# Optimization experiments

Hardware: AMD Instinct MI355X
Metric: run time of the kernel (lower is better)

The kernel has to match this reference:

```python
import jax, jax.numpy as jnp
import numpy as np

B, C, INTER, H, W = 4, 256, 128, 64, 64
EPS = 1e-5

def conv1x1(x, w, b):
    # x: [B,Cin,H,W], w: [Cout,Cin], b: [Cout]
    return jnp.einsum('bchw,oc->bohw', x, w) + b[None, :, None, None]

def setup_inputs() -> dict:
    key = jax.random.key(0)
    ks = jax.random.split(key, 12)
    sc_in = 1.0 / np.sqrt(C)
    sc_int = 1.0 / np.sqrt(INTER)
    return {
        'x': jax.random.normal(ks[0], (B, C, H, W), dtype=jnp.float32),
        'g_w': jax.random.normal(ks[1], (INTER, C), dtype=jnp.float32) * sc_in,
        'g_b': jax.random.normal(ks[2], (INTER,), dtype=jnp.float32) * 0.01,
        'theta_w': jax.random.normal(ks[3], (INTER, C), dtype=jnp.float32) * sc_in,
        'theta_b': jax.random.normal(ks[4], (INTER,), dtype=jnp.float32) * 0.01,
        'phi_w': jax.random.normal(ks[5], (INTER, C), dtype=jnp.float32) * sc_in,
        'phi_b': jax.random.normal(ks[6], (INTER,), dtype=jnp.float32) * 0.01,
        'w_w': jax.random.normal(ks[7], (C, INTER), dtype=jnp.float32) * sc_int,
        'w_b': jax.random.normal(ks[8], (C,), dtype=jnp.float32) * 0.01,
        'gamma': jax.random.normal(ks[9], (C,), dtype=jnp.float32) * 0.1 + 1.0,
        'beta': jax.random.normal(ks[10], (C,), dtype=jnp.float32) * 0.1,
    }

def reference(x, g_w, g_b, theta_w, theta_b, phi_w, phi_b, w_w, w_b, gamma, beta):
    b, c, h, w = x.shape
    n = h * w
    g_x = conv1x1(x, g_w, g_b).reshape(b, INTER, n).transpose(0, 2, 1)      # [b,n,d]
    theta_x = conv1x1(x, theta_w, theta_b).reshape(b, INTER, n).transpose(0, 2, 1)  # [b,n,d]
    phi_x = conv1x1(x, phi_w, phi_b).reshape(b, INTER, n)                   # [b,d,n]
    f = jnp.einsum('bnd,bdm->bnm', theta_x, phi_x)                          # [b,n,n]
    f_div_c = jax.nn.softmax(f, axis=-1)
    y = jnp.einsum('bnm,bmd->bnd', f_div_c, g_x)                            # [b,n,d]
    y = y.transpose(0, 2, 1).reshape(b, INTER, h, w)                        # [b,d,h,w]
    w_y = conv1x1(y, w_w, w_b)                                              # [b,c,h,w]
    # BatchNorm2d (training mode: batch statistics, biased variance)
    mean = jnp.mean(w_y, axis=(0, 2, 3), keepdims=True)
    var = jnp.var(w_y, axis=(0, 2, 3), keepdims=True)
    bn = (w_y - mean) * jax.lax.rsqrt(var + EPS)
    bn = bn * gamma[None, :, None, None] + beta[None, :, None, None]
    return bn + x
```

## Files before the change

kernel.cpp:

```cpp
#include <hip/hip_runtime.h>

#define B_ 4
#define C_ 256
#define D_ 128
#define N_ 4096
#define BN_ 16384

typedef unsigned short u16t;
typedef _Float16 f16t;
typedef f16t f16x8 __attribute__((ext_vector_type(8)));
typedef f16t f16x4 __attribute__((ext_vector_type(4)));
typedef float f32x4 __attribute__((ext_vector_type(4)));

static __device__ __forceinline__ u16t f2h(float f) {
  f16t h = (f16t)f; u16t u; __builtin_memcpy(&u, &h, 2); return u;
}
static __device__ __forceinline__ float h2f(u16t u) {
  f16t h; __builtin_memcpy(&h, &u, 2); return (float)h;
}

static __device__ __forceinline__ void gld_lds16(const u16t* g, u16t* l) {
  __builtin_amdgcn_global_load_lds(
      (const __attribute__((address_space(1))) void*)g,
      (__attribute__((address_space(3))) void*)l, 16, 0, 0);
}

__global__ __launch_bounds__(256) void prep_w(const float* __restrict__ th_w,
                                              const float* __restrict__ ph_w,
                                              const float* __restrict__ th_b,
                                              const float* __restrict__ ph_b,
                                              const float* __restrict__ g_w,
                                              const float* __restrict__ w_w,
                                              u16t* __restrict__ Wc, u16t* __restrict__ gwc,
                                              u16t* __restrict__ wwc, float* __restrict__ bc,
                                              float* __restrict__ stats) {
  const int idx = blockIdx.x * 256 + threadIdx.x;
  if (idx < 65536) {
    const int j = idx >> 8, c = idx & 255;
    const float v = (j < 128) ? th_w[j * 256 + c] : ph_w[(j - 128) * 256 + c];
    Wc[idx] = f2h(v);
  } else if (idx < 98304) {
    const int i = idx - 65536;
    gwc[i] = f2h(g_w[i]);
  } else if (idx < 131072) {
    const int i = idx - 98304;
    wwc[i] = f2h(w_w[i]);
  } else if (idx < 131328) {
    const int j = idx - 131072;
    bc[j] = (j < 128) ? th_b[j] : ph_b[j - 128];
  } else if (idx < 131840) {
    stats[idx - 131328] = 0.f;
  }
}

__global__ __launch_bounds__(256) void transpose_x(const float* __restrict__ x,
                                                   u16t* __restrict__ xT) {
  __shared__ u16t t[32][33];
  const int b = blockIdx.z, c0 = blockIdx.y * 32, n0 = blockIdx.x * 32;
  const int tid = threadIdx.x;
  {
    const int cl = tid >> 3, n4 = (tid & 7) * 4;
    const float4 v = *(const float4*)(x + ((size_t)b * C_ + c0 + cl) * N_ + n0 + n4);
    t[n4 + 0][cl] = f2h(v.x);
    t[n4 + 1][cl] = f2h(v.y);
    t[n4 + 2][cl] = f2h(v.z);
    t[n4 + 3][cl] = f2h(v.w);
  }
  __syncthreads();
  {
    const int nl = tid >> 3, c4 = (tid & 7) * 4;
    unsigned int lo = (unsigned int)t[nl][c4 + 0] | ((unsigned int)t[nl][c4 + 1] << 16);
    unsigned int hi = (unsigned int)t[nl][c4 + 2] | ((unsigned int)t[nl][c4 + 3] << 16);
    uint2 o; o.x = lo; o.y = hi;
    *(uint2*)(xT + ((size_t)b * N_ + n0 + nl) * C_ + c0 + c4) = o;
  }
}

__global__ __launch_bounds__(256)
void gemm_qkv(const u16t* __restrict__ xT, const u16t* __restrict__ Wc,
              const u16t* __restrict__ gwc, const float* __restrict__ bc,
              const float* __restrict__ g_b, u16t* __restrict__ QKo,
              u16t* __restrict__ Vo) {
  __shared__ __attribute__((aligned(16))) u16t lA[128 * 40];
  __shared__ __attribute__((aligned(16))) u16t lB[128 * 40];
  const int z = blockIdx.z, bx = blockIdx.x;
  const u16t* xTb = xT + (size_t)z * N_ * C_;
  const u16t* A; const u16t* B; u16t* Cb; int ldc, m0, j0, colb;
  const float* bias;
  if (bx < 64) {
    A = xTb; B = Wc; Cb = QKo + (size_t)z * N_ * 256; ldc = 256;
    m0 = (bx >> 1) * 128; j0 = (bx & 1) * 128; bias = bc; colb = 1;
  } else {
    A = gwc; B = xTb; Cb = Vo + (size_t)z * D_ * N_; ldc = N_;
    m0 = 0; j0 = (bx - 64) * 128; bias = g_b; colb = 0;
  }
  const int tid = threadIdx.x, lane = tid & 63, wave = tid >> 6;
  const int quad = lane >> 4, l16 = lane & 15;
  const int wm = wave & 1, wj = wave >> 1;

  const f32x4 zero = {0.f, 0.f, 0.f, 0.f};
  f32x4 acc[4][4];
#pragma unroll
  for (int mi = 0; mi < 4; ++mi)
#pragma unroll
    for (int ji = 0; ji < 4; ++ji) acc[mi][ji] = zero;

  for (int k0 = 0; k0 < 256; k0 += 32) {
#pragma unroll
    for (int rr = 0; rr < 2; ++rr) {
      const int idx = rr * 256 + tid;
      const int row = idx >> 2, sg = idx & 3;
      *(uint4*)&lA[row * 40 + sg * 8] = *(const uint4*)(A + (size_t)(m0 + row) * 256 + k0 + sg * 8);
      *(uint4*)&lB[row * 40 + sg * 8] = *(const uint4*)(B + (size_t)(j0 + row) * 256 + k0 + sg * 8);
    }
    __syncthreads();
    f16x8 af[4], bfr[4];
#pragma unroll
    for (int i = 0; i < 4; ++i)
      af[i] = *(const f16x8*)&lA[(wm * 64 + i * 16 + l16) * 40 + quad * 8];
#pragma unroll
    for (int i = 0; i < 4; ++i)
      bfr[i] = *(const f16x8*)&lB[(wj * 64 + i * 16 + l16) * 40 + quad * 8];
#pragma unroll
    for (int mi = 0; mi < 4; ++mi)
#pragma unroll
      for (int ji = 0; ji < 4; ++ji)
        acc[mi][ji] = __builtin_amdgcn_mfma_f32_16x16x32_f16(af[mi], bfr[ji], acc[mi][ji], 0, 0, 0);
    __syncthreads();
  }

  float cb[4];
  if (colb) {
#pragma unroll
    for (int ji = 0; ji < 4; ++ji) cb[ji] = bias[j0 + wj * 64 + ji * 16 + l16];
  }
#pragma unroll
  for (int mi = 0; mi < 4; ++mi) {
#pragma unroll
    for (int r = 0; r < 4; ++r) {
      const int row = m0 + wm * 64 + mi * 16 + quad * 4 + r;
      const float rb = colb ? 0.f : bias[row];
#pragma unroll
      for (int ji = 0; ji < 4; ++ji) {
        const int col = j0 + wj * 64 + ji * 16 + l16;
        const float v = acc[mi][ji][r] + (colb ? cb[ji] : rb);
        Cb[(size_t)row * ldc + col] = f2h(v);
      }
    }
  }
}

__global__ __launch_bounds__(256, 2)
void attn(const u16t* __restrict__ QK, const u16t* __restrict__ V,
          u16t* __restrict__ On0, u16t* __restrict__ On1, float* __restrict__ ml) {
  const int b = blockIdx.y;
  const int split = blockIdx.z;
  const int n0 = blockIdx.x * 128;
  const int kv0 = split * (N_ / 4);
  const int tid = threadIdx.x, lane = tid & 63, wave = tid >> 6;
  const int quad = lane >> 4, l16 = lane & 15;
  const int x7 = l16 & 7;
  __shared__ __attribute__((aligned(16))) u16t Ks[2][64 * 128];
  __shared__ __attribute__((aligned(16))) u16t Vs[2][128 * 64];
  const u16t* QKb = QK + (size_t)b * N_ * 256;
  const u16t* Vb  = V  + (size_t)b * D_ * N_;

  const int krow_l = lane >> 4, kchunk_l = lane & 15;
  const int vrow_l = lane >> 3, vchunk_l = lane & 7;

  f16x8 qf[2][4];
#pragma unroll
  for (int qi = 0; qi < 2; ++qi) {
    const u16t* qrow = QKb + (size_t)(n0 + wave * 32 + qi * 16 + l16) * 256;
#pragma unroll
    for (int kc = 0; kc < 4; ++kc)
      qf[qi][kc] = *(const f16x8*)(qrow + kc * 32 + quad * 8);
  }

  const f32x4 zero = {0.f, 0.f, 0.f, 0.f};
  f32x4 o[2][8];
#pragma unroll
  for (int qi = 0; qi < 2; ++qi)
#pragma unroll
    for (int db = 0; db < 8; ++db) o[qi][db] = zero;
  float m[2] = {-1e30f, -1e30f}, l[2] = {0.f, 0.f};

#pragma unroll
  for (int i = 0; i < 4; ++i) {
    const int krow = (wave * 4 + i) * 4 + krow_l;
    const int kcl = kchunk_l ^ (krow & 7);
    gld_lds16(QKb + (size_t)(kv0 + krow) * 256 + 128 + kcl * 8,
              &Ks[0][(wave * 4 + i) * 512]);
  }
#pragma unroll
  for (int i = 0; i < 4; ++i) {
    const int vrow = (wave * 4 + i) * 8 + vrow_l;
    const int vcl = vchunk_l ^ (vrow & 7);
    gld_lds16(Vb + (size_t)vrow * N_ + kv0 + vcl * 8,
              &Vs[0][(wave * 4 + i) * 512]);
  }
  __syncthreads();

  int cur = 0;
  for (int it = 0; it < 16; ++it) {
    if (it < 15) {
      const int kvn = kv0 + (it + 1) * 64;
#pragma unroll
      for (int i = 0; i < 4; ++i) {
        const int krow = (wave * 4 + i) * 4 + krow_l;
        const int kcl = kchunk_l ^ (krow & 7);
        gld_lds16(QKb + (size_t)(kvn + krow) * 256 + 128 + kcl * 8,
                  &Ks[cur ^ 1][(wave * 4 + i) * 512]);
      }
#pragma unroll
      for (int i = 0; i < 4; ++i) {
        const int vrow = (wave * 4 + i) * 8 + vrow_l;
        const int vcl = vchunk_l ^ (vrow & 7);
        gld_lds16(Vb + (size_t)vrow * N_ + kvn + vcl * 8,
                  &Vs[cur ^ 1][(wave * 4 + i) * 512]);
      }
    }

    const u16t* KsC = &Ks[cur][0];
    const u16t* VsC = &Vs[cur][0];

    f32x4 s[2][4];
#pragma unroll
    for (int qi = 0; qi < 2; ++qi)
#pragma unroll
      for (int ci = 0; ci < 4; ++ci) s[qi][ci] = zero;
#pragma unroll
    for (int kc = 0; kc < 4; ++kc) {
#pragma unroll
      for (int ci = 0; ci < 4; ++ci) {
        f16x8 kf = *(const f16x8*)&KsC[(ci * 16 + l16) * 128 + (((kc * 4 + quad) ^ x7) << 3)];
        s[0][ci] = __builtin_amdgcn_mfma_f32_16x16x32_f16(kf, qf[0][kc], s[0][ci], 0, 0, 0);
        s[1][ci] = __builtin_amdgcn_mfma_f32_16x16x32_f16(kf, qf[1][kc], s[1][ci], 0, 0, 0);
      }
    }

    float al[2];
    f16x4 pb[2][4];
#pragma unroll
    for (int qi = 0; qi < 2; ++qi) {
      float mx = s[qi][0][0];
#pragma unroll
      for (int ci = 0; ci < 4; ++ci)
#pragma unroll
        for (int r = 0; r < 4; ++r) mx = fmaxf(mx, s[qi][ci][r]);
      mx = fmaxf(mx, __shfl_xor(mx, 16));
      mx = fmaxf(mx, __shfl_xor(mx, 32));
      const float mnew = fmaxf(m[qi], mx);
      al[qi] = __expf(m[qi] - mnew);
      float psum = 0.f;
#pragma unroll
      for (int ci = 0; ci < 4; ++ci) {
#pragma unroll
        for (int r = 0; r < 4; ++r) {
          const float p = __expf(s[qi][ci][r] - mnew);
          psum += p;
          pb[qi][ci][r] = (f16t)p;
        }
      }
      psum += __shfl_xor(psum, 16);
      psum += __shfl_xor(psum, 32);
      l[qi] = l[qi] * al[qi] + psum;
      m[qi] = mnew;
    }

#pragma unroll
    for (int qi = 0; qi < 2; ++qi)
#pragma unroll
      for (int db = 0; db < 8; ++db) {
#pragma unroll
        for (int r = 0; r < 4; ++r) o[qi][db][r] *= al[qi];
      }
#pragma unroll
    for (int ci = 0; ci < 4; ++ci) {
#pragma unroll
      for (int db = 0; db < 8; ++db) {
        f16x4 av = *(const f16x4*)&VsC[(db * 16 + l16) * 64 +
                                       (((ci * 2 + (quad >> 1)) ^ x7) << 3) + (quad & 1) * 4];
        o[0][db] = __builtin_amdgcn_mfma_f32_16x16x16f16(av, pb[0][ci], o[0][db], 0, 0, 0);
        o[1][db] = __builtin_amdgcn_mfma_f32_16x16x16f16(av, pb[1][ci], o[1][db], 0, 0, 0);
      }
    }
    __syncthreads();
    cur ^= 1;
  }

  u16t* Onb = (split < 2) ? On0 : On1;
  const int sp = split & 1;
#pragma unroll
  for (int qi = 0; qi < 2; ++qi) {
    const int q = n0 + wave * 32 + qi * 16 + l16;
    const float inv = 1.0f / l[qi];
    u16t* yrow = Onb + (((size_t)sp * B_ + b) * N_ + q) * D_;
#pragma unroll
    for (int db = 0; db < 8; ++db) {
      f16x4 pk;
#pragma unroll
      for (int r = 0; r < 4; ++r) pk[r] = (f16t)(o[qi][db][r] * inv);
      *(f16x4*)(yrow + db * 16 + quad * 4) = pk;
    }
    if (quad == 0) {
      float* mlp = ml + ((size_t)split * BN_ + (size_t)b * N_ + q) * 2;
      mlp[0] = m[qi]; mlp[1] = l[qi];
    }
  }
}

__global__ __launch_bounds__(256)
void gemm_wy(const u16t* __restrict__ wwc, const u16t* __restrict__ O0,
             const u16t* __restrict__ O2, const float* __restrict__ ml,
             u16t* __restrict__ wy, const float* __restrict__ w_b,
             float* __restrict__ stats) {
  __shared__ __attribute__((aligned(16))) u16t lA[128 * 40];
  __shared__ __attribute__((aligned(16))) u16t lB[128 * 40];
  __shared__ float wrow[128][4];
  const int z = blockIdx.z;
  const int m0 = blockIdx.y * 128, j0 = blockIdx.x * 128;
  const int tid = threadIdx.x, lane = tid & 63, wave = tid >> 6;
  const int quad = lane >> 4, l16 = lane & 15;
  const int wm = wave & 1, wj = wave >> 1;

  if (tid < 128) {
    const int q = j0 + tid;
    float mv[4], lv[4], mstar = -1e30f;
#pragma unroll
    for (int s = 0; s < 4; ++s) {
      mv[s] = ml[((size_t)s * BN_ + (size_t)z * N_ + q) * 2];
      lv[s] = ml[((size_t)s * BN_ + (size_t)z * N_ + q) * 2 + 1];
      mstar = fmaxf(mstar, mv[s]);
    }
    float w[4], wsum = 0.f;
#pragma unroll
    for (int s = 0; s < 4; ++s) { w[s] = __expf(mv[s] - mstar) * lv[s]; wsum += w[s]; }
    const float inv = 1.0f / wsum;
#pragma unroll
    for (int s = 0; s < 4; ++s) wrow[tid][s] = w[s] * inv;
  }
  __syncthreads();

  const size_t halfO = (size_t)BN_ * D_;
  const f32x4 zero = {0.f, 0.f, 0.f, 0.f};
  f32x4 acc[4][4];
#pragma unroll
  for (int mi = 0; mi < 4; ++mi)
#pragma unroll
    for (int ji = 0; ji < 4; ++ji) acc[mi][ji] = zero;

  for (int k0 = 0; k0 < 128; k0 += 32) {
#pragma unroll
    for (int rr = 0; rr < 2; ++rr) {
      const int idx = rr * 256 + tid;
      const int row = idx >> 2, sg = idx & 3;
      *(uint4*)&lA[row * 40 + sg * 8] = *(const uint4*)(wwc + (size_t)(m0 + row) * 128 + k0 + sg * 8);
      const float w0 = wrow[row][0], w1 = wrow[row][1];
      const float w2 = wrow[row][2], w3 = wrow[row][3];
      const size_t base = ((size_t)z * N_ + j0 + row) * D_ + k0 + sg * 8;
      uint4 a0 = *(const uint4*)(O0 + base);
      uint4 a1 = *(const uint4*)(O0 + halfO + base);
      uint4 a2 = *(const uint4*)(O2 + base);
      uint4 a3 = *(const uint4*)(O2 + halfO + base);
      const unsigned* p0 = &a0.x; const unsigned* p1 = &a1.x;
      const unsigned* p2 = &a2.x; const unsigned* p3 = &a3.x;
      uint4 y; unsigned* py = &y.x;
#pragma unroll
      for (int i = 0; i < 4; ++i) {
        const float lo = w0 * h2f((u16t)(p0[i] & 0xffff)) + w1 * h2f((u16t)(p1[i] & 0xffff)) +
                         w2 * h2f((u16t)(p2[i] & 0xffff)) + w3 * h2f((u16t)(p3[i] & 0xffff));
        const float hi = w0 * h2f((u16t)(p0[i] >> 16)) + w1 * h2f((u16t)(p1[i] >> 16)) +
                         w2 * h2f((u16t)(p2[i] >> 16)) + w3 * h2f((u16t)(p3[i] >> 16));
        py[i] = (unsigned)f2h(lo) | ((unsigned)f2h(hi) << 16);
      }
      *(uint4*)&lB[row * 40 + sg * 8] = y;
    }
    __syncthreads();
    f16x8 af[4], bfr[4];
#pragma unroll
    for (int i = 0; i < 4; ++i)
      af[i] = *(const f16x8*)&lA[(wm * 64 + i * 16 + l16) * 40 + quad * 8];
#pragma unroll
    for (int i = 0; i < 4; ++i)
      bfr[i] = *(const f16x8*)&lB[(wj * 64 + i * 16 + l16) * 40 + quad * 8];
#pragma unroll
    for (int mi = 0; mi < 4; ++mi)
#pragma unroll
      for (int ji = 0; ji < 4; ++ji)
        acc[mi][ji] = __builtin_amdgcn_mfma_f32_16x16x32_f16(af[mi], bfr[ji], acc[mi][ji], 0, 0, 0);
    __syncthreads();
  }

#pragma unroll
  for (int mi = 0; mi < 4; ++mi) {
#pragma unroll
    for (int r = 0; r < 4; ++r) {
      const int row = m0 + wm * 64 + mi * 16 + quad * 4 + r;
      const float rb = w_b[row];
      float s1 = 0.f, s2 = 0.f;
#pragma unroll
      for (int ji = 0; ji < 4; ++ji) {
        const int col = j0 + wj * 64 + ji * 16 + l16;
        const float v = acc[mi][ji][r] + rb;
        wy[(size_t)z * C_ * N_ + (size_t)row * N_ + col] = f2h(v);
        s1 += v; s2 += v * v;
      }
      s1 += __shfl_xor(s1, 1); s1 += __shfl_xor(s1, 2);
      s1 += __shfl_xor(s1, 4); s1 += __shfl_xor(s1, 8);
      s2 += __shfl_xor(s2, 1); s2 += __shfl_xor(s2, 2);
      s2 += __shfl_xor(s2, 4); s2 += __shfl_xor(s2, 8);
      if (l16 == 0) {
        atomicAdd(&stats[row], s1);
        atomicAdd(&stats[256 + row], s2);
      }
    }
  }
}

__global__ __launch_bounds__(256) void bn_fin(const u16t* __restrict__ wy,
                                              const float* __restrict__ x,
                                              const float* __restrict__ stats,
                                              const float* __restrict__ gamma,
                                              const float* __restrict__ beta,
                                              float* __restrict__ out) {
  const int b = blockIdx.z, c = blockIdx.y;
  const int n4 = (blockIdx.x * 256 + threadIdx.x) * 4;
  const size_t off = ((size_t)b * C_ + c) * N_ + n4;
  const float inv_n = 1.0f / 16384.0f;
  const float mean = stats[c] * inv_n;
  const float var = stats[256 + c] * inv_n - mean * mean;
  const float rs = rsqrtf(var + 1e-5f);
  const float g = gamma[c], bt = beta[c];
  const uint2 wv = *(const uint2*)(wy + off);
  const float4 xv = *(const float4*)(x + off);
  float4 ov;
  ov.x = (h2f((u16t)(wv.x & 0xffff)) - mean) * rs * g + bt + xv.x;
  ov.y = (h2f((u16t)(wv.x >> 16))    - mean) * rs * g + bt + xv.y;
  ov.z = (h2f((u16t)(wv.y & 0xffff)) - mean) * rs * g + bt + xv.z;
  ov.w = (h2f((u16t)(wv.y >> 16))    - mean) * rs * g + bt + xv.w;
  *(float4*)(out + off) = ov;
}

extern "C" void kernel_launch(void* const* d_in, const int* in_sizes, int n_in,
                              void* d_out, int out_size, void* d_ws, size_t ws_size,
                              hipStream_t stream) {
  const float* x     = (const float*)d_in[0];
  const float* g_w   = (const float*)d_in[1];
  const float* g_b   = (const float*)d_in[2];
  const float* th_w  = (const float*)d_in[3];
  const float* th_b  = (const float*)d_in[4];
  const float* ph_w  = (const float*)d_in[5];
  const float* ph_b  = (const float*)d_in[6];
  const float* w_w   = (const float*)d_in[7];
  const float* w_b   = (const float*)d_in[8];
  const float* gamma = (const float*)d_in[9];
  const float* beta  = (const float*)d_in[10];
  float* out = (float*)d_out;
  char* ws = (char*)d_ws;

  u16t* O0  = (u16t*)(ws);
  u16t* QK  = (u16t*)(ws + 8388608);
  u16t* wy  = (u16t*)(ws + 8388608);
  u16t* V   = (u16t*)(ws + 16777216);
  u16t* Wc  = (u16t*)(ws + 20971520);
  u16t* gwc = (u16t*)(ws + 21102592);
  u16t* wwc = (u16t*)(ws + 21168128);
  float* bc = (float*)(ws + 21233664);
  float* stats = (float*)(ws + 21234688);
  float* ml = (float*)(ws + 21236736);
  u16t* O2 = (u16t*)d_out;

  prep_w<<<dim3(515), dim3(256), 0, stream>>>(th_w, ph_w, th_b, ph_b, g_w, w_w,
                                              Wc, gwc, wwc, bc, stats);
  transpose_x<<<dim3(128, 8, B_), dim3(256), 0, stream>>>(x, (u16t*)ws);

  gemm_qkv<<<dim3(96, 1, B_), dim3(256), 0, stream>>>(
      (u16t*)ws, Wc, gwc, bc, g_b, QK, V);

  attn<<<dim3(32, B_, 4), dim3(256), 0, stream>>>(QK, V, O0, O2, ml);

  gemm_wy<<<dim3(32, 2, B_), dim3(256), 0, stream>>>(wwc, O0, O2, ml, wy, w_b, stats);

  bn_fin<<<dim3(4, 256, B_), dim3(256), 0, stream>>>(wy, x, stats, gamma, beta, out);
}
```

Measured before the change: 205.9 us.

## Restructure gemm_wy to load full K upfront and halve column tile

```diff
diff --git a/kernel.cpp b/kernel.cpp
--- a/kernel.cpp
+++ b/kernel.cpp
@@ -315,81 +315,105 @@
              const u16t* __restrict__ O2, const float* __restrict__ ml,
              u16t* __restrict__ wy, const float* __restrict__ w_b,
              float* __restrict__ stats) {
-  __shared__ __attribute__((aligned(16))) u16t lA[128 * 40];
-  __shared__ __attribute__((aligned(16))) u16t lB[128 * 40];
-  __shared__ float wrow[128][4];
+  __shared__ __attribute__((aligned(16))) u16t lA[4][128 * 40];
+  __shared__ __attribute__((aligned(16))) u16t lB[4][64 * 40];
+  __shared__ float wrow[64][4];
   const int z = blockIdx.z;
-  const int m0 = blockIdx.y * 128, j0 = blockIdx.x * 128;
+  const int m0 = blockIdx.y * 128, j0 = blockIdx.x * 64;
   const int tid = threadIdx.x, lane = tid & 63, wave = tid >> 6;
   const int quad = lane >> 4, l16 = lane & 15;
   const int wm = wave & 1, wj = wave >> 1;
-
-  if (tid < 128) {
+  const size_t halfO = (size_t)BN_ * D_;
+
+  uint4 b0[4], b1[4], b2[4], b3[4];
+#pragma unroll
+  for (int cs = 0; cs < 4; ++cs) {
+    const int cid = cs * 256 + tid;
+    const int row = cid >> 4, sg = cid & 15;
+    const size_t base = ((size_t)z * N_ + j0 + row) * D_ + sg * 8;
+    b0[cs] = *(const uint4*)(O0 + base);
+    b1[cs] = *(const uint4*)(O0 + halfO + base);
+    b2[cs] = *(const uint4*)(O2 + base);
+    b3[cs] = *(const uint4*)(O2 + halfO + base);
+  }
+  uint4 aw[8];
+#pragma unroll
+  for (int as = 0; as < 8; ++as) {
+    const int cid = as * 256 + tid;
+    const int row = cid >> 4, sg = cid & 15;
+    aw[as] = *(const uint4*)(wwc + (size_t)(m0 + row) * 128 + sg * 8);
+  }
+  float mlv[8];
+  if (tid < 64) {
     const int q = j0 + tid;
-    float mv[4], lv[4], mstar = -1e30f;
 #pragma unroll
     for (int s = 0; s < 4; ++s) {
-      mv[s] = ml[((size_t)s * BN_ + (size_t)z * N_ + q) * 2];
-      lv[s] = ml[((size_t)s * BN_ + (size_t)z * N_ + q) * 2 + 1];
-      mstar = fmaxf(mstar, mv[s]);
-    }
+      mlv[2 * s]     = ml[((size_t)s * BN_ + (size_t)z * N_ + q) * 2];
+      mlv[2 * s + 1] = ml[((size_t)s * BN_ + (size_t)z * N_ + q) * 2 + 1];
+    }
+  }
+
+  if (tid < 64) {
+    float mstar = -1e30f;
+#pragma unroll
+    for (int s = 0; s < 4; ++s) mstar = fmaxf(mstar, mlv[2 * s]);
     float w[4], wsum = 0.f;
 #pragma unroll
-    for (int s = 0; s < 4; ++s) { w[s] = __expf(mv[s] - mstar) * lv[s]; wsum += w[s]; }
+    for (int s = 0; s < 4; ++s) { w[s] = __expf(mlv[2 * s] - mstar) * mlv[2 * s + 1]; wsum += w[s]; }
     const float inv = 1.0f / wsum;
 #pragma unroll
     for (int s = 0; s < 4; ++s) wrow[tid][s] = w[s] * inv;
   }
+
+#pragma unroll
+  for (int as = 0; as < 8; ++as) {
+    const int cid = as * 256 + tid;
+    const int row = cid >> 4, sg = cid & 15;
+    *(uint4*)&lA[sg >> 2][row * 40 + (sg & 3) * 8] = aw[as];
+  }
   __syncthreads();
 
-  const size_t halfO = (size_t)BN_ * D_;
+#pragma unroll
+  for (int cs = 0; cs < 4; ++cs) {
+    const int cid = cs * 256 + tid;
+    const int row = cid >> 4, sg = cid & 15;
+    const float w0 = wrow[row][0], w1 = wrow[row][1];
+    const float w2 = wrow[row][2], w3 = wrow[row][3];
+    const unsigned* p0 = &b0[cs].x; const unsigned* p1 = &b1[cs].x;
+    const unsigned* p2 = &b2[cs].x; const unsigned* p3 = &b3[cs].x;
+    uint4 y; unsigned* py = &y.x;
+#pragma unroll
+    for (int i = 0; i < 4; ++i) {
+      const float lo = w0 * h2f((u16t)(p0[i] & 0xffff)) + w1 * h2f((u16t)(p1[i] & 0xffff)) +
+                       w2 * h2f((u16t)(p2[i] & 0xffff)) + w3 * h2f((u16t)(p3[i] & 0xffff));
+      const float hi = w0 * h2f((u16t)(p0[i] >> 16)) + w1 * h2f((u16t)(p1[i] >> 16)) +
+                       w2 * h2f((u16t)(p2[i] >> 16)) + w3 * h2f((u16t)(p3[i] >> 16));
+      py[i] = (unsigned)f2h(lo) | ((unsigned)f2h(hi) << 16);
+    }
+    *(uint4*)&lB[sg >> 2][row * 40 + (sg & 3) * 8] = y;
+  }
+  __syncthreads();
+
   const f32x4 zero = {0.f, 0.f, 0.f, 0.f};
-  f32x4 acc[4][4];
+  f32x4 acc[4][2];
 #pragma unroll
   for (int mi = 0; mi < 4; ++mi)
 #pragma unroll
-    for (int ji = 0; ji < 4; ++ji) acc[mi][ji] = zero;
-
-  for (int k0 = 0; k0 < 128; k0 += 32) {
-#pragma unroll
-    for (int rr = 0; rr < 2; ++rr) {
-      const int idx = rr * 256 + tid;
-      const int row = idx >> 2, sg = idx & 3;
-      *(uint4*)&lA[row * 40 + sg * 8] = *(const uint4*)(wwc + (size_t)(m0 + row) * 128 + k0 + sg * 8);
-      const float w0 = wrow[row][0], w1 = wrow[row][1];
-      const float w2 = wrow[row][2], w3 = wrow[row][3];
-      const size_t base = ((size_t)z * N_ + j0 + row) * D_ + k0 + sg * 8;
-      uint4 a0 = *(const uint4*)(O0 + base);
-      uint4 a1 = *(const uint4*)(O0 + halfO + base);
-      uint4 a2 = *(const uint4*)(O2 + base);
-      uint4 a3 = *(const uint4*)(O2 + halfO + base);
-      const unsigned* p0 = &a0.x; const unsigned* p1 = &a1.x;
-      const unsigned* p2 = &a2.x; const unsigned* p3 = &a3.x;
-      uint4 y; unsigned* py = &y.x;
-#pragma unroll
-      for (int i = 0; i < 4; ++i) {
-        const float lo = w0 * h2f((u16t)(p0[i] & 0xffff)) + w1 * h2f((u16t)(p1[i] & 0xffff)) +
-                         w2 * h2f((u16t)(p2[i] & 0xffff)) + w3 * h2f((u16t)(p3[i] & 0xffff));
-        const float hi = w0 * h2f((u16t)(p0[i] >> 16)) + w1 * h2f((u16t)(p1[i] >> 16)) +
-                         w2 * h2f((u16t)(p2[i] >> 16)) + w3 * h2f((u16t)(p3[i] >> 16));
-        py[i] = (unsigned)f2h(lo) | ((unsigned)f2h(hi) << 16);
-      }
-      *(uint4*)&lB[row * 40 + sg * 8] = y;
-    }
-    __syncthreads();
-    f16x8 af[4], bfr[4];
+    for (int ji = 0; ji < 2; ++ji) acc[mi][ji] = zero;
+#pragma unroll
+  for (int kc = 0; kc < 4; ++kc) {
+    f16x8 af[4], bfr[2];
 #pragma unroll
     for (int i = 0; i < 4; ++i)
-      af[i] = *(const f16x8*)&lA[(wm * 64 + i * 16 + l16) * 40 + quad * 8];
-#pragma unroll
-    for (int i = 0; i < 4; ++i)
-      bfr[i] = *(const f16x8*)&lB[(wj * 64 + i * 16 + l16) * 40 + quad * 8];
+      af[i] = *(const f16x8*)&lA[kc][(wm * 64 + i * 16 + l16) * 40 + quad * 8];
+#pragma unroll
+    for (int i = 0; i < 2; ++i)
+      bfr[i] = *(const f16x8*)&lB[kc][(wj * 32 + i * 16 + l16) * 40 + quad * 8];
 #pragma unroll
     for (int mi = 0; mi < 4; ++mi)
 #pragma unroll
-      for (int ji = 0; ji < 4; ++ji)
+      for (int ji = 0; ji < 2; ++ji)
         acc[mi][ji] = __builtin_amdgcn_mfma_f32_16x16x32_f16(af[mi], bfr[ji], acc[mi][ji], 0, 0, 0);
-    __syncthreads();
   }
 
 #pragma unroll
@@ -400,8 +424,8 @@
       const float rb = w_b[row];
       float s1 = 0.f, s2 = 0.f;
 #pragma unroll
-      for (int ji = 0; ji < 4; ++ji) {
-        const int col = j0 + wj * 64 + ji * 16 + l16;
+      for (int ji = 0; ji < 2; ++ji) {
+        const int col = j0 + wj * 32 + ji * 16 + l16;
         const float v = acc[mi][ji][r] + rb;
         wy[(size_t)z * C_ * N_ + (size_t)row * N_ + col] = f2h(v);
         s1 += v; s2 += v * v;
@@ -480,7 +504,7 @@
 
   attn<<<dim3(32, B_, 4), dim3(256), 0, stream>>>(QK, V, O0, O2, ml);
 
-  gemm_wy<<<dim3(32, 2, B_), dim3(256), 0, stream>>>(wwc, O0, O2, ml, wy, w_b, stats);
+  gemm_wy<<<dim3(64, 2, B_), dim3(256), 0, stream>>>(wwc, O0, O2, ml, wy, w_b, stats);
 
   bn_fin<<<dim3(4, 256, B_), dim3(256), 0, stream>>>(wy, x, stats, gamma, beta, out);
 }
```

After: 232.5 us. 12.9% more time.
